# Performance work log

Measured on AMD Instinct MI355X. Metric: run time of the kernel, lower is better.

The kernel has to match this reference:

```python
import jax, jax.numpy as jnp
import numpy as np

N = 50000      # nodes
E = 800000     # edges (avg degree 16)
H = 128        # hidden_channels
F = 128        # num_filters
G = 50         # num_gaussians
L = 6          # num_interactions
CUT = 10.0     # cutoff
H2 = H // 2
OUT = 12


def ssp(x):
    # ShiftedSoftplus: softplus(x) - log(2)
    return jax.nn.softplus(x) - jnp.log(2.0)


def setup_inputs() -> dict:
    key = jax.random.key(0)
    ks = jax.random.split(key, 16)
    s = 0.05
    x_atoms = jax.random.randint(ks[0], (N,), 0, 100)
    edge_index = jax.random.randint(ks[1], (2, E), 0, N)
    edge_attr = jax.random.uniform(ks[2], (E,), minval=0.05, maxval=CUT)
    return {
        "x_atoms": x_atoms,
        "edge_index": edge_index,
        "edge_attr": edge_attr,
        "embedding": jax.random.normal(ks[3], (100, H)) * s,
        # per-interaction stacked params [L, ...]
        "mlp_w1": jax.random.normal(ks[4], (L, G, F)) * s,
        "mlp_b1": jnp.zeros((L, F)),
        "mlp_w2": jax.random.normal(ks[5], (L, F, F)) * s,
        "mlp_b2": jnp.zeros((L, F)),
        "conv1_w": jax.random.normal(ks[6], (L, H, F)) * s,   # CFConv.lin1 (no bias)
        "conv2_w": jax.random.normal(ks[7], (L, F, H)) * s,   # CFConv.lin2
        "conv2_b": jnp.zeros((L, H)),
        "int_lin_w": jax.random.normal(ks[8], (L, H, H)) * s,  # InteractionBlock.lin
        "int_lin_b": jnp.zeros((L, H)),
        # head
        "lin1_w": jax.random.normal(ks[9], (H, H2)) * s,
        "lin1_b": jnp.zeros((H2,)),
        "lin2_w": jax.random.normal(ks[10], (H2, H2)) * s,
        "lin2_b": jnp.zeros((H2,)),
        "readout_w": jax.random.normal(ks[11], (H2, OUT)) * s,
        "readout_b": jnp.zeros((OUT,)),
    }


def reference(x_atoms, edge_index, edge_attr, embedding,
              mlp_w1, mlp_b1, mlp_w2, mlp_b2,
              conv1_w, conv2_w, conv2_b, int_lin_w, int_lin_b,
              lin1_w, lin1_b, lin2_w, lin2_b, readout_w, readout_b):
    h = embedding[x_atoms]  # [N, H]

    # Gaussian smearing of distances -> [E, G]
    offset = jnp.linspace(0.0, CUT, G)
    coeff = -0.5 / (offset[1] - offset[0]) ** 2
    ed = jnp.exp(coeff * (edge_attr[:, None] - offset) ** 2)

    # cosine cutoff weight per edge
    C = 0.5 * (jnp.cos(edge_attr * jnp.pi / CUT) + 1.0)  # [E]

    src = edge_index[0]
    dst = edge_index[1]

    for l in range(L):
        # filter network on expanded distances -> [E, F]
        W = ssp(ed @ mlp_w1[l] + mlp_b1[l]) @ mlp_w2[l] + mlp_b2[l]
        W = W * C[:, None]
        xf = h @ conv1_w[l]                     # [N, F]
        msg = xf[src] * W                        # gather + modulate, [E, F]
        agg = jax.ops.segment_sum(msg, dst, num_segments=N)  # scatter-add, [N, F]
        v = agg @ conv2_w[l] + conv2_b[l]        # [N, H]
        v = ssp(v)
        v = v @ int_lin_w[l] + int_lin_b[l]
        h = h + v                                # residual

    h = ssp(h @ lin1_w + lin1_b)
    h = h @ lin2_w + lin2_b
    h_agg = jnp.sum(h, axis=0, keepdims=True)    # [1, H2]
    return h_agg @ readout_w + readout_b         # [1, OUT]
```

## Files before the change

kernel.cpp:

```cpp
#include <hip/hip_runtime.h>
#include <hip/hip_bf16.h>
#include <math.h>

#define NN 50000
#define EE 800000
#define HH 128
#define FF 128
#define GG 50
#define LL 6
#define H2D 64
#define OUT_DIM 12
#define NK 4096
#define NBLK 782
#define SB 196
#define NBUK 196

typedef __bf16 bf16;
typedef __attribute__((ext_vector_type(8))) __bf16 bf16x8;
typedef __attribute__((ext_vector_type(4))) __bf16 bf16x4;
typedef __attribute__((ext_vector_type(4))) float f32x4;
typedef __attribute__((ext_vector_type(4))) unsigned u32x4;

#define DEV __device__ __forceinline__

DEV float sspf(float x) {
    return fmaxf(x, 0.f) + __logf(1.f + __expf(-fabsf(x))) - 0.69314718055994531f;
}

DEV f32x4 mfma16(bf16x8 a, bf16x8 b, f32x4 c) {
    return __builtin_amdgcn_mfma_f32_16x16x32_bf16(a, b, c, 0, 0, 0);
}

DEV float blo(unsigned u) { return __uint_as_float(u << 16); }
DEV float bhi(unsigned u) { return __uint_as_float(u & 0xffff0000u); }

struct PrepArgs {
    const float *conv1_w, *conv2_w, *int_lin_w, *mlp_w1, *mlp_w2, *lin1_w, *lin2_w;
    bf16 *c1t, *c2t, *ilt, *w1t, *w2t, *l1t, *l2t;
};

__global__ void prep_kernel(PrepArgs p) {
    int j = blockIdx.x;
    const float* src = nullptr; bf16* dst = nullptr; int R = 0, C = 0, K = 0;
    if (j < 30) {
        int l = j / 5, m = j % 5;
        switch (m) {
            case 0: src = p.conv1_w + l * HH * FF;   dst = p.c1t + l * FF * HH;  R = HH; C = FF; K = HH; break;
            case 1: src = p.conv2_w + l * FF * HH;   dst = p.c2t + l * HH * FF;  R = FF; C = HH; K = FF; break;
            case 2: src = p.int_lin_w + l * HH * HH; dst = p.ilt + l * HH * HH;  R = HH; C = HH; K = HH; break;
            case 3: src = p.mlp_w1 + l * GG * FF;    dst = p.w1t + l * FF * 64;  R = GG; C = FF; K = 64; break;
            case 4: src = p.mlp_w2 + l * FF * FF;    dst = p.w2t + l * FF * FF;  R = FF; C = FF; K = FF; break;
        }
    } else if (j == 30) { src = p.lin1_w; dst = p.l1t; R = HH;  C = H2D; K = HH; }
    else                { src = p.lin2_w; dst = p.l2t; R = H2D; C = H2D; K = H2D; }
    int total = C * K;
    for (int idx = threadIdx.x; idx < total; idx += blockDim.x) {
        int c = idx / K, r = idx - c * K;
        dst[idx] = (r < R) ? (bf16)src[r * C + c] : (bf16)0.f;
    }
}

__global__ __launch_bounds__(256) void table_kernel(const bf16* __restrict__ w1t,
                                                    const bf16* __restrict__ w2t,
                                                    const float* __restrict__ mlp_b1,
                                                    const float* __restrict__ mlp_b2,
                                                    bf16* __restrict__ tab) {
    __shared__ bf16 sW1[128 * 72];
    __shared__ bf16 sW2[128 * 136];
    __shared__ bf16 sT1[64 * 136];
    int tid = threadIdx.x;
    int l = blockIdx.x / 65, rb = blockIdx.x % 65;
    const bf16* W1 = w1t + (size_t)l * 128 * 64;
    const bf16* W2 = w2t + (size_t)l * 128 * 128;
    for (int idx = tid * 8; idx < 128 * 64; idx += 2048) {
        int n = idx >> 6, k = idx & 63;
        *(bf16x8*)&sW1[n * 72 + k] = *(const bf16x8*)(W1 + idx);
    }
    for (int idx = tid * 8; idx < 128 * 128; idx += 2048) {
        int n = idx >> 7, k = idx & 127;
        *(bf16x8*)&sW2[n * 136 + k] = *(const bf16x8*)(W2 + idx);
    }
    int w = tid >> 6, lane = tid & 63, ln = lane & 15, kg = lane >> 4;
    int rowt = rb * 64 + w * 16;
    float d1 = (float)min(rowt + ln, NK) * (10.f / NK);
    const float step = 10.f / 49.f;
    const float coeff = -0.5f / (step * step);
    __syncthreads();
    f32x4 acc[8] = {};
#pragma unroll
    for (int k0 = 0; k0 < 64; k0 += 32) {
        bf16x8 a;
#pragma unroll
        for (int jj = 0; jj < 8; jj++) {
            int g = k0 + kg * 8 + jj;
            float diff = d1 - g * step;
            float v = (g < GG) ? __expf(coeff * diff * diff) : 0.f;
            a[jj] = (bf16)v;
        }
#pragma unroll
        for (int t = 0; t < 8; t++) {
            bf16x8 b = *(const bf16x8*)&sW1[(t * 16 + ln) * 72 + k0 + kg * 8];
            acc[t] = mfma16(a, b, acc[t]);
        }
    }
    const float* b1 = mlp_b1 + l * FF;
#pragma unroll
    for (int t = 0; t < 8; t++) {
        int colt = t * 16 + ln;
        float bb = b1[colt];
#pragma unroll
        for (int r = 0; r < 4; r++)
            sT1[(w * 16 + kg * 4 + r) * 136 + colt] = (bf16)sspf(acc[t][r] + bb);
    }
    __syncthreads();
    f32x4 acc2[8] = {};
#pragma unroll
    for (int k0 = 0; k0 < 128; k0 += 32) {
        bf16x8 a = *(const bf16x8*)&sT1[(w * 16 + ln) * 136 + k0 + kg * 8];
#pragma unroll
        for (int t = 0; t < 8; t++) {
            bf16x8 b = *(const bf16x8*)&sW2[(t * 16 + ln) * 136 + k0 + kg * 8];
            acc2[t] = mfma16(a, b, acc2[t]);
        }
    }
    const float* b2 = mlp_b2 + l * FF;
    float Cw[4]; int rrow[4];
#pragma unroll
    for (int r = 0; r < 4; r++) {
        int rr = rowt + kg * 4 + r;
        rrow[r] = rr;
        float dd = (float)min(rr, NK) * (10.f / NK);
        Cw[r] = 0.5f * (cosf(dd * 0.31415926535897932f) + 1.f);
    }
#pragma unroll
    for (int t = 0; t < 8; t++) {
        int colt = t * 16 + ln;
        float bb = b2[colt];
#pragma unroll
        for (int r = 0; r < 4; r++) {
            if (rrow[r] <= NK)
                tab[((size_t)l * (NK + 1) + rrow[r]) * FF + colt] = (bf16)((acc2[t][r] + bb) * Cw[r]);
        }
    }
}

__global__ void hist_kernel(const int* __restrict__ eidx, int* __restrict__ hist) {
    int e = blockIdx.x * 256 + threadIdx.x;
    if (e < EE) atomicAdd(&hist[eidx[EE + e]], 1);
}

__global__ __launch_bounds__(256) void scanA_kernel(const int* __restrict__ hist,
                                                    int* __restrict__ bsum) {
    __shared__ int red[256];
    int t = threadIdx.x;
    int i = blockIdx.x * 256 + t;
    int v = (i < NN) ? hist[i] : 0;
    red[t] = v;
    __syncthreads();
    for (int off = 128; off > 0; off >>= 1) {
        if (t < off) red[t] += red[t + off];
        __syncthreads();
    }
    if (t == 0) bsum[blockIdx.x] = red[0];
}

__global__ __launch_bounds__(256) void scanB_kernel(int* __restrict__ bsum) {
    __shared__ int buf[256];
    int t = threadIdx.x;
    int v = (t < SB) ? bsum[t] : 0;
    buf[t] = v;
    __syncthreads();
    for (int off = 1; off < 256; off <<= 1) {
        int y = (t >= off) ? buf[t - off] : 0;
        __syncthreads();
        buf[t] += y;
        __syncthreads();
    }
    if (t < SB) bsum[t] = buf[t] - v;
}

__global__ __launch_bounds__(256) void scanC_kernel(const int* __restrict__ hist,
                                                    const int* __restrict__ bsum,
                                                    int* __restrict__ rs) {
    __shared__ int buf[256];
    int t = threadIdx.x;
    int i = blockIdx.x * 256 + t;
    int v = (i < NN) ? hist[i] : 0;
    buf[t] = v;
    __syncthreads();
    for (int off = 1; off < 256; off <<= 1) {
        int y = (t >= off) ? buf[t - off] : 0;
        __syncthreads();
        buf[t] += y;
        __syncthreads();
    }
    if (i < NN) rs[i] = buf[t] - v + bsum[blockIdx.x];
}

__global__ void bukinit_kernel(const int* __restrict__ rs, int* __restrict__ bucket_cur) {
    int b = threadIdx.x;
    if (b < NBUK) bucket_cur[b] = rs[b * 256];
}

__global__ __launch_bounds__(256) void scat1_kernel(const float* __restrict__ eattr,
                                                    const int* __restrict__ eidx,
                                                    int* __restrict__ bucket_cur,
                                                    int2* __restrict__ tmp8) {
    __shared__ int cnt[NBUK];
    __shared__ int res[NBUK];
    int t = threadIdx.x;
    for (int i = t; i < NBUK; i += 256) cnt[i] = 0;
    __syncthreads();
    int e0 = blockIdx.x * 4096;
    int pv[16], dd[16], bk[16];
#pragma unroll
    for (int i = 0; i < 16; i++) {
        int e = e0 + i * 256 + t;
        if (e < EE) {
            int d = eidx[EE + e];
            int k = (int)(eattr[e] * ((float)NK / 10.f) + 0.5f);
            k = min(k, NK);
            pv[i] = k | (eidx[e] << 13);
            dd[i] = d;
            bk[i] = d >> 8;
            atomicAdd(&cnt[bk[i]], 1);
        } else bk[i] = -1;
    }
    __syncthreads();
    for (int i = t; i < NBUK; i += 256) {
        int c = cnt[i];
        res[i] = (c > 0) ? atomicAdd(&bucket_cur[i], c) : 0;
        cnt[i] = 0;
    }
    __syncthreads();
#pragma unroll
    for (int i = 0; i < 16; i++) {
        if (bk[i] >= 0) {
            int rank = atomicAdd(&cnt[bk[i]], 1);
            int2 v; v.x = pv[i]; v.y = dd[i];
            tmp8[res[bk[i]] + rank] = v;
        }
    }
}

__global__ __launch_bounds__(256) void scat2_kernel(const int* __restrict__ rs,
                                                    const int2* __restrict__ tmp8,
                                                    int* __restrict__ es) {
    __shared__ int off[256];
    __shared__ int loc[256];
    int b = blockIdx.x, t = threadIdx.x;
    int nb0 = b * 256;
    int nnb = min(256, NN - nb0);
    int base = rs[nb0];
    int end = (nb0 + 256 < NN) ? rs[nb0 + 256] : EE;
    loc[t] = 0;
    if (t < nnb) off[t] = rs[nb0 + t] - base;
    __syncthreads();
    for (int e = base + t; e < end; e += 256) {
        int2 v = tmp8[e];
        int nl = v.y - nb0;
        int rank = atomicAdd(&loc[nl], 1);
        es[base + off[nl] + rank] = v.x;
    }
}

__global__ void embed_kernel(const int* __restrict__ x_atoms, const float* __restrict__ emb,
                             bf16* __restrict__ hb) {
    int idx = blockIdx.x * blockDim.x + threadIdx.x;
    if (idx >= NN * 16) return;
    int n = idx >> 4, ch = idx & 15;
    int a = x_atoms[n];
    const float* ep = emb + a * HH + ch * 8;
    f32x4 v0 = *(const f32x4*)ep;
    f32x4 v1 = *(const f32x4*)(ep + 4);
    bf16x8 vb;
#pragma unroll
    for (int q = 0; q < 4; q++) { vb[q] = (bf16)v0[q]; vb[q + 4] = (bf16)v1[q]; }
    *(bf16x8*)(hb + n * HH + ch * 8) = vb;
}

__global__ __launch_bounds__(256) void xf_kernel(const bf16* __restrict__ hb,
                                                 const bf16* __restrict__ c1t,
                                                 bf16* __restrict__ xf) {
    __shared__ bf16 sB[128 * 136];
    int tid = threadIdx.x;
    for (int idx = tid * 8; idx < 128 * 128; idx += 2048) {
        int n = idx >> 7, k = idx & 127;
        *(bf16x8*)&sB[n * 136 + k] = *(const bf16x8*)(c1t + idx);
    }
    int w = tid >> 6, lane = tid & 63, ln = lane & 15, kg = lane >> 4;
    int rowt = blockIdx.x * 64 + w * 16;
    int arow = min(rowt + ln, NN - 1);
    __syncthreads();
    f32x4 acc[8] = {};
#pragma unroll
    for (int k0 = 0; k0 < 128; k0 += 32) {
        bf16x8 a = *(const bf16x8*)(hb + arow * HH + k0 + kg * 8);
#pragma unroll
        for (int t = 0; t < 8; t++) {
            bf16x8 b = *(const bf16x8*)&sB[(t * 16 + ln) * 136 + k0 + kg * 8];
            acc[t] = mfma16(a, b, acc[t]);
        }
    }
#pragma unroll
    for (int t = 0; t < 8; t++) {
        int colt = t * 16 + ln;
#pragma unroll
        for (int r = 0; r < 4; r++) {
            int orow = rowt + kg * 4 + r;
            if (orow < NN) xf[orow * FF + colt] = (bf16)acc[t][r];
        }
    }
}

__global__ __launch_bounds__(256) void edge_kernel(const int* __restrict__ es,
                                                   const int* __restrict__ rs,
                                                   const int* __restrict__ hist,
                                                   const bf16* __restrict__ xf,
                                                   const bf16* __restrict__ tab,
                                                   bf16* __restrict__ aggb) {
    int tid = threadIdx.x;
    int w = tid >> 6, lane = tid & 63;
    int q = lane >> 4, cl = lane & 15;
    int n = blockIdx.x * 4 + w;
    int start = rs[n], deg = hist[n];
    float a0 = 0.f, a1 = 0.f, a2 = 0.f, a3 = 0.f;
    float a4 = 0.f, a5 = 0.f, a6 = 0.f, a7 = 0.f;
    for (int base = 0; base < deg; base += 64) {
        int cnt = min(deg - base, 64);
        int pv = (lane < cnt) ? es[start + base + lane] : 0;
        int iters = (cnt + 3) >> 2;
#pragma unroll 4
        for (int j = 0; j < iters; j++) {
            int jj = 4 * j + q;
            bool valid = jj < cnt;
            int v = __shfl(pv, jj);
            int k = v & 8191;
            int s = v >> 13;
            u32x4 tp = *(const u32x4*)(tab + (size_t)k * FF + 8 * cl);
            u32x4 xu = *(const u32x4*)(xf + (size_t)s * FF + 8 * cl);
            unsigned t0 = valid ? tp.x : 0u;
            unsigned t1 = valid ? tp.y : 0u;
            unsigned t2 = valid ? tp.z : 0u;
            unsigned t3 = valid ? tp.w : 0u;
            a0 = fmaf(blo(t0), blo(xu.x), a0);
            a1 = fmaf(bhi(t0), bhi(xu.x), a1);
            a2 = fmaf(blo(t1), blo(xu.y), a2);
            a3 = fmaf(bhi(t1), bhi(xu.y), a3);
            a4 = fmaf(blo(t2), blo(xu.z), a4);
            a5 = fmaf(bhi(t2), bhi(xu.z), a5);
            a6 = fmaf(blo(t3), blo(xu.w), a6);
            a7 = fmaf(bhi(t3), bhi(xu.w), a7);
        }
    }
    a0 += __shfl_xor(a0, 16); a0 += __shfl_xor(a0, 32);
    a1 += __shfl_xor(a1, 16); a1 += __shfl_xor(a1, 32);
    a2 += __shfl_xor(a2, 16); a2 += __shfl_xor(a2, 32);
    a3 += __shfl_xor(a3, 16); a3 += __shfl_xor(a3, 32);
    a4 += __shfl_xor(a4, 16); a4 += __shfl_xor(a4, 32);
    a5 += __shfl_xor(a5, 16); a5 += __shfl_xor(a5, 32);
    a6 += __shfl_xor(a6, 16); a6 += __shfl_xor(a6, 32);
    a7 += __shfl_xor(a7, 16); a7 += __shfl_xor(a7, 32);
    if (q == 0) {
        bf16x8 pk;
        pk[0] = (bf16)a0; pk[1] = (bf16)a1; pk[2] = (bf16)a2; pk[3] = (bf16)a3;
        pk[4] = (bf16)a4; pk[5] = (bf16)a5; pk[6] = (bf16)a6; pk[7] = (bf16)a7;
        *(bf16x8*)(aggb + (size_t)n * FF + 8 * cl) = pk;
    }
}

__global__ __launch_bounds__(256) void update_kernel(const bf16* __restrict__ aggb,
                                                     const bf16* __restrict__ c2t,
                                                     const float* __restrict__ c2b,
                                                     const bf16* __restrict__ ilt,
                                                     const float* __restrict__ ilb,
                                                     bf16* __restrict__ hb,
                                                     const bf16* __restrict__ c1n,
                                                     bf16* __restrict__ xf_out,
                                                     const bf16* __restrict__ l1t,
                                                     const float* __restrict__ l1b,
                                                     const bf16* __restrict__ l2t,
                                                     const float* __restrict__ l2b,
                                                     float* __restrict__ partial) {
    __shared__ bf16 sB[128 * 136];
    __shared__ bf16 sT[64 * 136];
    int tid = threadIdx.x;
    int w = tid >> 6, lane = tid & 63, ln = lane & 15, kg = lane >> 4;
    int rowt = blockIdx.x * 64 + w * 16;
    int nrow = rowt + ln;
    int arow = min(nrow, NN - 1);
    bool rowok = nrow < NN;
    bf16x4 hpre[8];
#pragma unroll
    for (int t = 0; t < 8; t++)
        hpre[t] = *(const bf16x4*)(hb + (size_t)arow * HH + t * 16 + kg * 4);
    for (int idx = tid * 8; idx < 128 * 128; idx += 2048) {
        int n = idx >> 7, k = idx & 127;
        *(bf16x8*)&sB[n * 136 + k] = *(const bf16x8*)(c2t + idx);
    }
    __syncthreads();
    f32x4 acc[8] = {};
#pragma unroll
    for (int k0 = 0; k0 < 128; k0 += 32) {
        bf16x8 bfrag = *(const bf16x8*)(aggb + (size_t)arow * FF + k0 + kg * 8);
#pragma unroll
        for (int t = 0; t < 8; t++) {
            bf16x8 afrag = *(const bf16x8*)&sB[(t * 16 + ln) * 136 + k0 + kg * 8];
            acc[t] = mfma16(afrag, bfrag, acc[t]);
        }
    }
#pragma unroll
    for (int t = 0; t < 8; t++) {
        f32x4 bb = *(const f32x4*)(c2b + t * 16 + kg * 4);
        bf16x4 pk;
#pragma unroll
        for (int r = 0; r < 4; r++) pk[r] = (bf16)sspf(acc[t][r] + bb[r]);
        *(bf16x4*)&sT[(w * 16 + ln) * 136 + t * 16 + kg * 4] = pk;
    }
    __syncthreads();
    for (int idx = tid * 8; idx < 128 * 128; idx += 2048) {
        int n = idx >> 7, k = idx & 127;
        *(bf16x8*)&sB[n * 136 + k] = *(const bf16x8*)(ilt + idx);
    }
    __syncthreads();
    f32x4 acc2[8] = {};
#pragma unroll
    for (int k0 = 0; k0 < 128; k0 += 32) {
        bf16x8 bfrag = *(const bf16x8*)&sT[(w * 16 + ln) * 136 + k0 + kg * 8];
#pragma unroll
        for (int t = 0; t < 8; t++) {
            bf16x8 afrag = *(const bf16x8*)&sB[(t * 16 + ln) * 136 + k0 + kg * 8];
            acc2[t] = mfma16(afrag, bfrag, acc2[t]);
        }
    }
    bool is_last = (c1n == nullptr);
#pragma unroll
    for (int t = 0; t < 8; t++) {
        f32x4 bb = *(const f32x4*)(ilb + t * 16 + kg * 4);
        bf16x4 pk;
#pragma unroll
        for (int r = 0; r < 4; r++)
            pk[r] = (bf16)((float)hpre[t][r] + acc2[t][r] + bb[r]);
        if (rowok && !is_last) *(bf16x4*)(hb + (size_t)nrow * HH + t * 16 + kg * 4) = pk;
        *(bf16x4*)&sT[(w * 16 + ln) * 136 + t * 16 + kg * 4] = pk;
    }
    if (!is_last) {
        __syncthreads();
        for (int idx = tid * 8; idx < 128 * 128; idx += 2048) {
            int n = idx >> 7, k = idx & 127;
            *(bf16x8*)&sB[n * 136 + k] = *(const bf16x8*)(c1n + idx);
        }
        __syncthreads();
        f32x4 acc3[8] = {};
#pragma unroll
        for (int k0 = 0; k0 < 128; k0 += 32) {
            bf16x8 bfrag = *(const bf16x8*)&sT[(w * 16 + ln) * 136 + k0 + kg * 8];
#pragma unroll
            for (int t = 0; t < 8; t++) {
                bf16x8 afrag = *(const bf16x8*)&sB[(t * 16 + ln) * 136 + k0 + kg * 8];
                acc3[t] = mfma16(afrag, bfrag, acc3[t]);
            }
        }
#pragma unroll
        for (int t = 0; t < 8; t++) {
            bf16x4 pk;
#pragma unroll
            for (int r = 0; r < 4; r++) pk[r] = (bf16)acc3[t][r];
            if (rowok) *(bf16x4*)(xf_out + (size_t)nrow * FF + t * 16 + kg * 4) = pk;
        }
    } else {
        __syncthreads();
        for (int idx = tid * 8; idx < 64 * 128; idx += 2048) {
            int n = idx >> 7, k = idx & 127;
            *(bf16x8*)&sB[n * 136 + k] = *(const bf16x8*)(l1t + idx);
        }
        __syncthreads();
        f32x4 acch[4] = {};
#pragma unroll
        for (int k0 = 0; k0 < 128; k0 += 32) {
            bf16x8 a = *(const bf16x8*)&sT[(w * 16 + ln) * 136 + k0 + kg * 8];
#pragma unroll
            for (int t = 0; t < 4; t++) {
                bf16x8 b = *(const bf16x8*)&sB[(t * 16 + ln) * 136 + k0 + kg * 8];
                acch[t] = mfma16(a, b, acch[t]);
            }
        }
#pragma unroll
        for (int t = 0; t < 4; t++) {
            int colt = t * 16 + ln;
            float bb = l1b[colt];
#pragma unroll
            for (int r = 0; r < 4; r++)
                sT[(w * 16 + kg * 4 + r) * 136 + colt] = (bf16)sspf(acch[t][r] + bb);
        }
        __syncthreads();
        for (int idx = tid * 8; idx < 64 * 64; idx += 2048) {
            int n = idx >> 6, k = idx & 63;
            *(bf16x8*)&sB[n * 136 + k] = *(const bf16x8*)(l2t + idx);
        }
        __syncthreads();
        f32x4 acc2h[4] = {};
#pragma unroll
        for (int k0 = 0; k0 < 64; k0 += 32) {
            bf16x8 a = *(const bf16x8*)&sT[(w * 16 + ln) * 136 + k0 + kg * 8];
#pragma unroll
            for (int t = 0; t < 4; t++) {
                bf16x8 b = *(const bf16x8*)&sB[(t * 16 + ln) * 136 + k0 + kg * 8];
                acc2h[t] = mfma16(a, b, acc2h[t]);
            }
        }
        __syncthreads();
        float* sPart = (float*)sT;
#pragma unroll
        for (int t = 0; t < 4; t++) {
            int colt = t * 16 + ln;
            float bb = l2b[colt];
            float v = 0.f;
#pragma unroll
            for (int r = 0; r < 4; r++) {
                int orow = rowt + kg * 4 + r;
                if (orow < NN) v += acc2h[t][r] + bb;
            }
            v += __shfl_xor(v, 16);
            v += __shfl_xor(v, 32);
            if (kg == 0) sPart[w * 64 + colt] = v;
        }
        __syncthreads();
        if (tid < 64) {
            float s = sPart[tid] + sPart[64 + tid] + sPart[128 + tid] + sPart[192 + tid];
            partial[blockIdx.x * 64 + tid] = s;
        }
    }
}

__global__ __launch_bounds__(64) void final_kernel(const float* __restrict__ partial,
                                                   const float* __restrict__ rw,
                                                   const float* __restrict__ rb,
                                                   float* __restrict__ out) {
    __shared__ float sv[64];
    int j = threadIdx.x;
    float s = 0.f;
    for (int b = 0; b < NBLK; b++) s += partial[b * 64 + j];
    sv[j] = s;
    __syncthreads();
    if (j < OUT_DIM) {
        float o = rb[j];
        for (int i = 0; i < H2D; i++) o += sv[i] * rw[i * OUT_DIM + j];
        out[j] = o;
    }
}

extern "C" void kernel_launch(void* const* d_in, const int* in_sizes, int n_in,
                              void* d_out, int out_size, void* d_ws, size_t ws_size,
                              hipStream_t stream) {
    const int*   x_atoms    = (const int*)d_in[0];
    const int*   edge_index = (const int*)d_in[1];
    const float* edge_attr  = (const float*)d_in[2];
    const float* embedding  = (const float*)d_in[3];
    const float* mlp_w1     = (const float*)d_in[4];
    const float* mlp_b1     = (const float*)d_in[5];
    const float* mlp_w2     = (const float*)d_in[6];
    const float* mlp_b2     = (const float*)d_in[7];
    const float* conv1_w    = (const float*)d_in[8];
    const float* conv2_w    = (const float*)d_in[9];
    const float* conv2_b    = (const float*)d_in[10];
    const float* int_lin_w  = (const float*)d_in[11];
    const float* int_lin_b  = (const float*)d_in[12];
    const float* lin1_w     = (const float*)d_in[13];
    const float* lin1_b     = (const float*)d_in[14];
    const float* lin2_w     = (const float*)d_in[15];
    const float* lin2_b     = (const float*)d_in[16];
    const float* readout_w  = (const float*)d_in[17];
    const float* readout_b  = (const float*)d_in[18];

    char* ws = (char*)d_ws;
    bf16*  hb      = (bf16*)(ws + 0);
    bf16*  xfA     = (bf16*)(ws + 12800000);
    bf16*  xfB     = (bf16*)(ws + 25600000);
    bf16*  aggb    = (bf16*)(ws + 38400000);
    float* partial = (float*)(ws + 51200000);
    size_t wb = 51400192;
    bf16* c1t = (bf16*)(ws + wb);
    bf16* c2t = (bf16*)(ws + wb + 196608);
    bf16* ilt = (bf16*)(ws + wb + 393216);
    bf16* w1t = (bf16*)(ws + wb + 589824);
    bf16* w2t = (bf16*)(ws + wb + 688128);
    bf16* l1t = (bf16*)(ws + wb + 884736);
    bf16* l2t = (bf16*)(ws + wb + 901120);
    int*   d_hist = (int*)(ws + 52309504);
    int*   d_rs   = (int*)(ws + 52509504);
    int*   d_bcur = (int*)(ws + 52709504);
    int*   d_bsum = (int*)(ws + 52710528);
    int*   d_es   = (int*)(ws + 52711552);
    bf16*  tab    = (bf16*)(ws + 55911552);
    int2*  d_tmp8 = (int2*)(ws + 62204544);

    PrepArgs pa = { conv1_w, conv2_w, int_lin_w, mlp_w1, mlp_w2, lin1_w, lin2_w,
                    c1t, c2t, ilt, w1t, w2t, l1t, l2t };
    prep_kernel<<<32, 256, 0, stream>>>(pa);
    table_kernel<<<LL * 65, 256, 0, stream>>>(w1t, w2t, mlp_b1, mlp_b2, tab);
    embed_kernel<<<NN * 16 / 256, 256, 0, stream>>>(x_atoms, embedding, hb);

    hipMemsetAsync(d_hist, 0, NN * 4, stream);
    hist_kernel<<<(EE + 255) / 256, 256, 0, stream>>>(edge_index, d_hist);
    scanA_kernel<<<SB, 256, 0, stream>>>(d_hist, d_bsum);
    scanB_kernel<<<1, 256, 0, stream>>>(d_bsum);
    scanC_kernel<<<SB, 256, 0, stream>>>(d_hist, d_bsum, d_rs);
    bukinit_kernel<<<1, 256, 0, stream>>>(d_rs, d_bcur);
    scat1_kernel<<<NBUK, 256, 0, stream>>>(edge_attr, edge_index, d_bcur, d_tmp8);
    scat2_kernel<<<NBUK, 256, 0, stream>>>(d_rs, d_tmp8, d_es);

    xf_kernel<<<NBLK, 256, 0, stream>>>(hb, c1t, xfA);
    bf16* xf_in = xfA;
    bf16* xf_out = xfB;
    for (int l = 0; l < LL; l++) {
        edge_kernel<<<NN / 4, 256, 0, stream>>>(d_es, d_rs, d_hist, xf_in,
                                                tab + (size_t)l * (NK + 1) * FF, aggb);
        const bf16* c1n = (l + 1 < LL) ? (c1t + (size_t)(l + 1) * FF * HH) : nullptr;
        update_kernel<<<NBLK, 256, 0, stream>>>(aggb, c2t + (size_t)l * HH * FF,
                                                conv2_b + l * HH,
                                                ilt + (size_t)l * HH * HH, int_lin_b + l * HH,
                                                hb, c1n, xf_out,
                                                l1t, lin1_b, l2t, lin2_b, partial);
        bf16* tmp = xf_in; xf_in = xf_out; xf_out = tmp;
    }
    final_kernel<<<1, 64, 0, stream>>>(partial, readout_w, readout_b, (float*)d_out);
}
```

Measured before the change: 587.5 us.

## Remap edge kernel to 16 lanes per node and fuse embed into xf

The edge aggregation kernel now gives each node 16 threads, each walking the full edge list serially with unroll 2, in place of a 64-lane wavefront that split edges four ways and reduced with cross-lane shuffles. This removes the shuffle-based reduction and the padded, masked iterations for low-degree nodes, and packs 16 nodes into each block. The cost is a serial dependency chain per thread over about 16 edges, which relies on other wavefronts to hide latency. Separately, the embedding lookup is fused into the first xf GEMM kernel, and the bucket-cursor init is folded into scanC, which removes two launches.

After: 594.1 us. Within noise of the previous version (+1.1%).

```diff
diff --git a/kernel.cpp b/kernel.cpp
--- a/kernel.cpp
+++ b/kernel.cpp
@@ -181,7 +181,8 @@
 
 __global__ __launch_bounds__(256) void scanC_kernel(const int* __restrict__ hist,
                                                     const int* __restrict__ bsum,
-                                                    int* __restrict__ rs) {
+                                                    int* __restrict__ rs,
+                                                    int* __restrict__ bucket_cur) {
     __shared__ int buf[256];
     int t = threadIdx.x;
     int i = blockIdx.x * 256 + t;
@@ -194,12 +195,11 @@
         buf[t] += y;
         __syncthreads();
     }
-    if (i < NN) rs[i] = buf[t] - v + bsum[blockIdx.x];
-}
-
-__global__ void bukinit_kernel(const int* __restrict__ rs, int* __restrict__ bucket_cur) {
-    int b = threadIdx.x;
-    if (b < NBUK) bucket_cur[b] = rs[b * 256];
+    if (i < NN) {
+        int ex = buf[t] - v + bsum[blockIdx.x];
+        rs[i] = ex;
+        if ((i & 255) == 0) bucket_cur[i >> 8] = ex;
+    }
 }
 
 __global__ __launch_bounds__(256) void scat1_kernel(const float* __restrict__ eattr,
@@ -264,24 +264,11 @@
     }
 }
 
-__global__ void embed_kernel(const int* __restrict__ x_atoms, const float* __restrict__ emb,
-                             bf16* __restrict__ hb) {
-    int idx = blockIdx.x * blockDim.x + threadIdx.x;
-    if (idx >= NN * 16) return;
-    int n = idx >> 4, ch = idx & 15;
-    int a = x_atoms[n];
-    const float* ep = emb + a * HH + ch * 8;
-    f32x4 v0 = *(const f32x4*)ep;
-    f32x4 v1 = *(const f32x4*)(ep + 4);
-    bf16x8 vb;
-#pragma unroll
-    for (int q = 0; q < 4; q++) { vb[q] = (bf16)v0[q]; vb[q + 4] = (bf16)v1[q]; }
-    *(bf16x8*)(hb + n * HH + ch * 8) = vb;
-}
-
-__global__ __launch_bounds__(256) void xf_kernel(const bf16* __restrict__ hb,
-                                                 const bf16* __restrict__ c1t,
-                                                 bf16* __restrict__ xf) {
+__global__ __launch_bounds__(256) void xf0_kernel(const int* __restrict__ x_atoms,
+                                                  const float* __restrict__ emb,
+                                                  const bf16* __restrict__ c1t,
+                                                  bf16* __restrict__ hb,
+                                                  bf16* __restrict__ xf) {
     __shared__ bf16 sB[128 * 136];
     int tid = threadIdx.x;
     for (int idx = tid * 8; idx < 128 * 128; idx += 2048) {
@@ -290,12 +277,21 @@
     }
     int w = tid >> 6, lane = tid & 63, ln = lane & 15, kg = lane >> 4;
     int rowt = blockIdx.x * 64 + w * 16;
-    int arow = min(rowt + ln, NN - 1);
+    int nrow = rowt + ln;
+    int arow = min(nrow, NN - 1);
+    bool rowok = nrow < NN;
+    int atom = x_atoms[arow];
     __syncthreads();
     f32x4 acc[8] = {};
 #pragma unroll
     for (int k0 = 0; k0 < 128; k0 += 32) {
-        bf16x8 a = *(const bf16x8*)(hb + arow * HH + k0 + kg * 8);
+        const float* ep = emb + (size_t)atom * HH + k0 + kg * 8;
+        f32x4 u0 = *(const f32x4*)ep;
+        f32x4 u1 = *(const f32x4*)(ep + 4);
+        bf16x8 a;
+#pragma unroll
+        for (int q = 0; q < 4; q++) { a[q] = (bf16)u0[q]; a[q + 4] = (bf16)u1[q]; }
+        if (rowok) *(bf16x8*)(hb + (size_t)nrow * HH + k0 + kg * 8) = a;
 #pragma unroll
         for (int t = 0; t < 8; t++) {
             bf16x8 b = *(const bf16x8*)&sB[(t * 16 + ln) * 136 + k0 + kg * 8];
@@ -320,53 +316,32 @@
                                                    const bf16* __restrict__ tab,
                                                    bf16* __restrict__ aggb) {
     int tid = threadIdx.x;
-    int w = tid >> 6, lane = tid & 63;
-    int q = lane >> 4, cl = lane & 15;
-    int n = blockIdx.x * 4 + w;
+    int qq = tid >> 4;
+    int cl = tid & 15;
+    int n = blockIdx.x * 16 + qq;
     int start = rs[n], deg = hist[n];
     float a0 = 0.f, a1 = 0.f, a2 = 0.f, a3 = 0.f;
     float a4 = 0.f, a5 = 0.f, a6 = 0.f, a7 = 0.f;
-    for (int base = 0; base < deg; base += 64) {
-        int cnt = min(deg - base, 64);
-        int pv = (lane < cnt) ? es[start + base + lane] : 0;
-        int iters = (cnt + 3) >> 2;
-#pragma unroll 4
-        for (int j = 0; j < iters; j++) {
-            int jj = 4 * j + q;
-            bool valid = jj < cnt;
-            int v = __shfl(pv, jj);
-            int k = v & 8191;
-            int s = v >> 13;
-            u32x4 tp = *(const u32x4*)(tab + (size_t)k * FF + 8 * cl);
-            u32x4 xu = *(const u32x4*)(xf + (size_t)s * FF + 8 * cl);
-            unsigned t0 = valid ? tp.x : 0u;
-            unsigned t1 = valid ? tp.y : 0u;
-            unsigned t2 = valid ? tp.z : 0u;
-            unsigned t3 = valid ? tp.w : 0u;
-            a0 = fmaf(blo(t0), blo(xu.x), a0);
-            a1 = fmaf(bhi(t0), bhi(xu.x), a1);
-            a2 = fmaf(blo(t1), blo(xu.y), a2);
-            a3 = fmaf(bhi(t1), bhi(xu.y), a3);
-            a4 = fmaf(blo(t2), blo(xu.z), a4);
-            a5 = fmaf(bhi(t2), bhi(xu.z), a5);
-            a6 = fmaf(blo(t3), blo(xu.w), a6);
-            a7 = fmaf(bhi(t3), bhi(xu.w), a7);
-        }
-    }
-    a0 += __shfl_xor(a0, 16); a0 += __shfl_xor(a0, 32);
-    a1 += __shfl_xor(a1, 16); a1 += __shfl_xor(a1, 32);
-    a2 += __shfl_xor(a2, 16); a2 += __shfl_xor(a2, 32);
-    a3 += __shfl_xor(a3, 16); a3 += __shfl_xor(a3, 32);
-    a4 += __shfl_xor(a4, 16); a4 += __shfl_xor(a4, 32);
-    a5 += __shfl_xor(a5, 16); a5 += __shfl_xor(a5, 32);
-    a6 += __shfl_xor(a6, 16); a6 += __shfl_xor(a6, 32);
-    a7 += __shfl_xor(a7, 16); a7 += __shfl_xor(a7, 32);
-    if (q == 0) {
-        bf16x8 pk;
-        pk[0] = (bf16)a0; pk[1] = (bf16)a1; pk[2] = (bf16)a2; pk[3] = (bf16)a3;
-        pk[4] = (bf16)a4; pk[5] = (bf16)a5; pk[6] = (bf16)a6; pk[7] = (bf16)a7;
-        *(bf16x8*)(aggb + (size_t)n * FF + 8 * cl) = pk;
-    }
+#pragma unroll 2
+    for (int i = 0; i < deg; i++) {
+        int v = es[start + i];
+        int k = v & 8191;
+        int s = v >> 13;
+        u32x4 tp = *(const u32x4*)(tab + (size_t)k * FF + 8 * cl);
+        u32x4 xu = *(const u32x4*)(xf + (size_t)s * FF + 8 * cl);
+        a0 = fmaf(blo(tp.x), blo(xu.x), a0);
+        a1 = fmaf(bhi(tp.x), bhi(xu.x), a1);
+        a2 = fmaf(blo(tp.y), blo(xu.y), a2);
+        a3 = fmaf(bhi(tp.y), bhi(xu.y), a3);
+        a4 = fmaf(blo(tp.z), blo(xu.z), a4);
+        a5 = fmaf(bhi(tp.z), bhi(xu.z), a5);
+        a6 = fmaf(blo(tp.w), blo(xu.w), a6);
+        a7 = fmaf(bhi(tp.w), bhi(xu.w), a7);
+    }
+    bf16x8 pk;
+    pk[0] = (bf16)a0; pk[1] = (bf16)a1; pk[2] = (bf16)a2; pk[3] = (bf16)a3;
+    pk[4] = (bf16)a4; pk[5] = (bf16)a5; pk[6] = (bf16)a6; pk[7] = (bf16)a7;
+    *(bf16x8*)(aggb + (size_t)n * FF + 8 * cl) = pk;
 }
 
 __global__ __launch_bounds__(256) void update_kernel(const bf16* __restrict__ aggb,
@@ -599,23 +574,21 @@
                     c1t, c2t, ilt, w1t, w2t, l1t, l2t };
     prep_kernel<<<32, 256, 0, stream>>>(pa);
     table_kernel<<<LL * 65, 256, 0, stream>>>(w1t, w2t, mlp_b1, mlp_b2, tab);
-    embed_kernel<<<NN * 16 / 256, 256, 0, stream>>>(x_atoms, embedding, hb);
 
     hipMemsetAsync(d_hist, 0, NN * 4, stream);
     hist_kernel<<<(EE + 255) / 256, 256, 0, stream>>>(edge_index, d_hist);
     scanA_kernel<<<SB, 256, 0, stream>>>(d_hist, d_bsum);
     scanB_kernel<<<1, 256, 0, stream>>>(d_bsum);
-    scanC_kernel<<<SB, 256, 0, stream>>>(d_hist, d_bsum, d_rs);
-    bukinit_kernel<<<1, 256, 0, stream>>>(d_rs, d_bcur);
+    scanC_kernel<<<SB, 256, 0, stream>>>(d_hist, d_bsum, d_rs, d_bcur);
     scat1_kernel<<<NBUK, 256, 0, stream>>>(edge_attr, edge_index, d_bcur, d_tmp8);
     scat2_kernel<<<NBUK, 256, 0, stream>>>(d_rs, d_tmp8, d_es);
 
-    xf_kernel<<<NBLK, 256, 0, stream>>>(hb, c1t, xfA);
+    xf0_kernel<<<NBLK, 256, 0, stream>>>(x_atoms, embedding, c1t, hb, xfA);
     bf16* xf_in = xfA;
     bf16* xf_out = xfB;
     for (int l = 0; l < LL; l++) {
-        edge_kernel<<<NN / 4, 256, 0, stream>>>(d_es, d_rs, d_hist, xf_in,
-                                                tab + (size_t)l * (NK + 1) * FF, aggb);
+        edge_kernel<<<NN / 16, 256, 0, stream>>>(d_es, d_rs, d_hist, xf_in,
+                                                 tab + (size_t)l * (NK + 1) * FF, aggb);
         const bf16* c1n = (l + 1 < LL) ? (c1t + (size_t)(l + 1) * FF * HH) : nullptr;
         update_kernel<<<NBLK, 256, 0, stream>>>(aggb, c2t + (size_t)l * HH * FF,
                                                 conv2_b + l * HH,
```

## Merge setup kernels into one cooperative persistent kernel with grid syncs

Applied to the files above, without the earlier changes.

Replaces the chain of roughly a dozen setup launches (weight prep, filter table, embedding, histogram, scans, bucket scatter, first xf GEMM) with a single cooperative kernel of 392 blocks that uses grid.sync between phases. Independent work such as the table GEMM and the scan partials, or the xf GEMM and the block-sum scan, runs in the same phase. The embedding lookup is folded into the xf GEMM, so the separate hb round trip is gone. The cost is several grid-wide barriers, about 70KB of static shared memory per block that limits residency, and a cooperative launch requirement.

After: 878.8 us. +49.6%, slower.

```diff
diff --git a/kernel.cpp b/kernel.cpp
--- a/kernel.cpp
+++ b/kernel.cpp
@@ -1,6 +1,9 @@
 #include <hip/hip_runtime.h>
+#include <hip/hip_cooperative_groups.h>
 #include <hip/hip_bf16.h>
 #include <math.h>
+
+namespace cg = cooperative_groups;
 
 #define NN 50000
 #define EE 800000
@@ -14,6 +17,7 @@
 #define NBLK 782
 #define SB 196
 #define NBUK 196
+#define NB 392
 
 typedef __bf16 bf16;
 typedef __attribute__((ext_vector_type(8))) __bf16 bf16x8;
@@ -34,44 +38,44 @@
 DEV float blo(unsigned u) { return __uint_as_float(u << 16); }
 DEV float bhi(unsigned u) { return __uint_as_float(u & 0xffff0000u); }
 
-struct PrepArgs {
+struct SetupArgs {
     const float *conv1_w, *conv2_w, *int_lin_w, *mlp_w1, *mlp_w2, *lin1_w, *lin2_w;
     bf16 *c1t, *c2t, *ilt, *w1t, *w2t, *l1t, *l2t;
+    const float *mlp_b1, *mlp_b2;
+    const int* edge_index; const float* edge_attr;
+    int* hist; int* bsum; int* rs; int* bcur;
+    int2* tmp8; int* es;
+    const int* x_atoms; const float* emb;
+    bf16* tab; bf16* hb; bf16* xf;
 };
 
-__global__ void prep_kernel(PrepArgs p) {
-    int j = blockIdx.x;
+DEV void prep_job(const SetupArgs& a, int j, int tid) {
     const float* src = nullptr; bf16* dst = nullptr; int R = 0, C = 0, K = 0;
     if (j < 30) {
         int l = j / 5, m = j % 5;
         switch (m) {
-            case 0: src = p.conv1_w + l * HH * FF;   dst = p.c1t + l * FF * HH;  R = HH; C = FF; K = HH; break;
-            case 1: src = p.conv2_w + l * FF * HH;   dst = p.c2t + l * HH * FF;  R = FF; C = HH; K = FF; break;
-            case 2: src = p.int_lin_w + l * HH * HH; dst = p.ilt + l * HH * HH;  R = HH; C = HH; K = HH; break;
-            case 3: src = p.mlp_w1 + l * GG * FF;    dst = p.w1t + l * FF * 64;  R = GG; C = FF; K = 64; break;
-            case 4: src = p.mlp_w2 + l * FF * FF;    dst = p.w2t + l * FF * FF;  R = FF; C = FF; K = FF; break;
-        }
-    } else if (j == 30) { src = p.lin1_w; dst = p.l1t; R = HH;  C = H2D; K = HH; }
-    else                { src = p.lin2_w; dst = p.l2t; R = H2D; C = H2D; K = H2D; }
+            case 0: src = a.conv1_w + l * HH * FF;   dst = a.c1t + l * FF * HH;  R = HH; C = FF; K = HH; break;
+            case 1: src = a.conv2_w + l * FF * HH;   dst = a.c2t + l * HH * FF;  R = FF; C = HH; K = FF; break;
+            case 2: src = a.int_lin_w + l * HH * HH; dst = a.ilt + l * HH * HH;  R = HH; C = HH; K = HH; break;
+            case 3: src = a.mlp_w1 + l * GG * FF;    dst = a.w1t + l * FF * 64;  R = GG; C = FF; K = 64; break;
+            case 4: src = a.mlp_w2 + l * FF * FF;    dst = a.w2t + l * FF * FF;  R = FF; C = FF; K = FF; break;
+        }
+    } else if (j == 30) { src = a.lin1_w; dst = a.l1t; R = HH;  C = H2D; K = HH; }
+    else                { src = a.lin2_w; dst = a.l2t; R = H2D; C = H2D; K = H2D; }
     int total = C * K;
-    for (int idx = threadIdx.x; idx < total; idx += blockDim.x) {
+    for (int idx = tid; idx < total; idx += 256) {
         int c = idx / K, r = idx - c * K;
         dst[idx] = (r < R) ? (bf16)src[r * C + c] : (bf16)0.f;
     }
 }
 
-__global__ __launch_bounds__(256) void table_kernel(const bf16* __restrict__ w1t,
-                                                    const bf16* __restrict__ w2t,
-                                                    const float* __restrict__ mlp_b1,
-                                                    const float* __restrict__ mlp_b2,
-                                                    bf16* __restrict__ tab) {
-    __shared__ bf16 sW1[128 * 72];
-    __shared__ bf16 sW2[128 * 136];
-    __shared__ bf16 sT1[64 * 136];
-    int tid = threadIdx.x;
-    int l = blockIdx.x / 65, rb = blockIdx.x % 65;
-    const bf16* W1 = w1t + (size_t)l * 128 * 64;
-    const bf16* W2 = w2t + (size_t)l * 128 * 128;
+DEV void table_job(const SetupArgs& a, int job, char* smem, int tid) {
+    bf16* sW1 = (bf16*)smem;
+    bf16* sW2 = (bf16*)(smem + 18432);
+    bf16* sT1 = (bf16*)(smem + 53248);
+    int l = job / 65, rb = job % 65;
+    const bf16* W1 = a.w1t + (size_t)l * 128 * 64;
+    const bf16* W2 = a.w2t + (size_t)l * 128 * 128;
     for (int idx = tid * 8; idx < 128 * 64; idx += 2048) {
         int n = idx >> 6, k = idx & 63;
         *(bf16x8*)&sW1[n * 72 + k] = *(const bf16x8*)(W1 + idx);
@@ -89,21 +93,21 @@
     f32x4 acc[8] = {};
 #pragma unroll
     for (int k0 = 0; k0 < 64; k0 += 32) {
-        bf16x8 a;
+        bf16x8 av;
 #pragma unroll
         for (int jj = 0; jj < 8; jj++) {
             int g = k0 + kg * 8 + jj;
             float diff = d1 - g * step;
             float v = (g < GG) ? __expf(coeff * diff * diff) : 0.f;
-            a[jj] = (bf16)v;
+            av[jj] = (bf16)v;
         }
 #pragma unroll
         for (int t = 0; t < 8; t++) {
             bf16x8 b = *(const bf16x8*)&sW1[(t * 16 + ln) * 72 + k0 + kg * 8];
-            acc[t] = mfma16(a, b, acc[t]);
-        }
-    }
-    const float* b1 = mlp_b1 + l * FF;
+            acc[t] = mfma16(av, b, acc[t]);
+        }
+    }
+    const float* b1 = a.mlp_b1 + l * FF;
 #pragma unroll
     for (int t = 0; t < 8; t++) {
         int colt = t * 16 + ln;
@@ -116,14 +120,14 @@
     f32x4 acc2[8] = {};
 #pragma unroll
     for (int k0 = 0; k0 < 128; k0 += 32) {
-        bf16x8 a = *(const bf16x8*)&sT1[(w * 16 + ln) * 136 + k0 + kg * 8];
+        bf16x8 av = *(const bf16x8*)&sT1[(w * 16 + ln) * 136 + k0 + kg * 8];
 #pragma unroll
         for (int t = 0; t < 8; t++) {
             bf16x8 b = *(const bf16x8*)&sW2[(t * 16 + ln) * 136 + k0 + kg * 8];
-            acc2[t] = mfma16(a, b, acc2[t]);
-        }
-    }
-    const float* b2 = mlp_b2 + l * FF;
+            acc2[t] = mfma16(av, b, acc2[t]);
+        }
+    }
+    const float* b2 = a.mlp_b2 + l * FF;
     float Cw[4]; int rrow[4];
 #pragma unroll
     for (int r = 0; r < 4; r++) {
@@ -139,167 +143,38 @@
 #pragma unroll
         for (int r = 0; r < 4; r++) {
             if (rrow[r] <= NK)
-                tab[((size_t)l * (NK + 1) + rrow[r]) * FF + colt] = (bf16)((acc2[t][r] + bb) * Cw[r]);
-        }
-    }
-}
-
-__global__ void hist_kernel(const int* __restrict__ eidx, int* __restrict__ hist) {
-    int e = blockIdx.x * 256 + threadIdx.x;
-    if (e < EE) atomicAdd(&hist[eidx[EE + e]], 1);
-}
-
-__global__ __launch_bounds__(256) void scanA_kernel(const int* __restrict__ hist,
-                                                    int* __restrict__ bsum) {
-    __shared__ int red[256];
-    int t = threadIdx.x;
-    int i = blockIdx.x * 256 + t;
-    int v = (i < NN) ? hist[i] : 0;
-    red[t] = v;
-    __syncthreads();
-    for (int off = 128; off > 0; off >>= 1) {
-        if (t < off) red[t] += red[t + off];
-        __syncthreads();
-    }
-    if (t == 0) bsum[blockIdx.x] = red[0];
-}
-
-__global__ __launch_bounds__(256) void scanB_kernel(int* __restrict__ bsum) {
-    __shared__ int buf[256];
-    int t = threadIdx.x;
-    int v = (t < SB) ? bsum[t] : 0;
-    buf[t] = v;
-    __syncthreads();
-    for (int off = 1; off < 256; off <<= 1) {
-        int y = (t >= off) ? buf[t - off] : 0;
-        __syncthreads();
-        buf[t] += y;
-        __syncthreads();
-    }
-    if (t < SB) bsum[t] = buf[t] - v;
-}
-
-__global__ __launch_bounds__(256) void scanC_kernel(const int* __restrict__ hist,
-                                                    const int* __restrict__ bsum,
-                                                    int* __restrict__ rs) {
-    __shared__ int buf[256];
-    int t = threadIdx.x;
-    int i = blockIdx.x * 256 + t;
-    int v = (i < NN) ? hist[i] : 0;
-    buf[t] = v;
-    __syncthreads();
-    for (int off = 1; off < 256; off <<= 1) {
-        int y = (t >= off) ? buf[t - off] : 0;
-        __syncthreads();
-        buf[t] += y;
-        __syncthreads();
-    }
-    if (i < NN) rs[i] = buf[t] - v + bsum[blockIdx.x];
-}
-
-__global__ void bukinit_kernel(const int* __restrict__ rs, int* __restrict__ bucket_cur) {
-    int b = threadIdx.x;
-    if (b < NBUK) bucket_cur[b] = rs[b * 256];
-}
-
-__global__ __launch_bounds__(256) void scat1_kernel(const float* __restrict__ eattr,
-                                                    const int* __restrict__ eidx,
-                                                    int* __restrict__ bucket_cur,
-                                                    int2* __restrict__ tmp8) {
-    __shared__ int cnt[NBUK];
-    __shared__ int res[NBUK];
-    int t = threadIdx.x;
-    for (int i = t; i < NBUK; i += 256) cnt[i] = 0;
-    __syncthreads();
-    int e0 = blockIdx.x * 4096;
-    int pv[16], dd[16], bk[16];
-#pragma unroll
-    for (int i = 0; i < 16; i++) {
-        int e = e0 + i * 256 + t;
-        if (e < EE) {
-            int d = eidx[EE + e];
-            int k = (int)(eattr[e] * ((float)NK / 10.f) + 0.5f);
-            k = min(k, NK);
-            pv[i] = k | (eidx[e] << 13);
-            dd[i] = d;
-            bk[i] = d >> 8;
-            atomicAdd(&cnt[bk[i]], 1);
-        } else bk[i] = -1;
-    }
-    __syncthreads();
-    for (int i = t; i < NBUK; i += 256) {
-        int c = cnt[i];
-        res[i] = (c > 0) ? atomicAdd(&bucket_cur[i], c) : 0;
-        cnt[i] = 0;
-    }
-    __syncthreads();
-#pragma unroll
-    for (int i = 0; i < 16; i++) {
-        if (bk[i] >= 0) {
-            int rank = atomicAdd(&cnt[bk[i]], 1);
-            int2 v; v.x = pv[i]; v.y = dd[i];
-            tmp8[res[bk[i]] + rank] = v;
-        }
-    }
-}
-
-__global__ __launch_bounds__(256) void scat2_kernel(const int* __restrict__ rs,
-                                                    const int2* __restrict__ tmp8,
-                                                    int* __restrict__ es) {
-    __shared__ int off[256];
-    __shared__ int loc[256];
-    int b = blockIdx.x, t = threadIdx.x;
-    int nb0 = b * 256;
-    int nnb = min(256, NN - nb0);
-    int base = rs[nb0];
-    int end = (nb0 + 256 < NN) ? rs[nb0 + 256] : EE;
-    loc[t] = 0;
-    if (t < nnb) off[t] = rs[nb0 + t] - base;
-    __syncthreads();
-    for (int e = base + t; e < end; e += 256) {
-        int2 v = tmp8[e];
-        int nl = v.y - nb0;
-        int rank = atomicAdd(&loc[nl], 1);
-        es[base + off[nl] + rank] = v.x;
-    }
-}
-
-__global__ void embed_kernel(const int* __restrict__ x_atoms, const float* __restrict__ emb,
-                             bf16* __restrict__ hb) {
-    int idx = blockIdx.x * blockDim.x + threadIdx.x;
-    if (idx >= NN * 16) return;
-    int n = idx >> 4, ch = idx & 15;
-    int a = x_atoms[n];
-    const float* ep = emb + a * HH + ch * 8;
-    f32x4 v0 = *(const f32x4*)ep;
-    f32x4 v1 = *(const f32x4*)(ep + 4);
-    bf16x8 vb;
-#pragma unroll
-    for (int q = 0; q < 4; q++) { vb[q] = (bf16)v0[q]; vb[q + 4] = (bf16)v1[q]; }
-    *(bf16x8*)(hb + n * HH + ch * 8) = vb;
-}
-
-__global__ __launch_bounds__(256) void xf_kernel(const bf16* __restrict__ hb,
-                                                 const bf16* __restrict__ c1t,
-                                                 bf16* __restrict__ xf) {
-    __shared__ bf16 sB[128 * 136];
-    int tid = threadIdx.x;
+                a.tab[((size_t)l * (NK + 1) + rrow[r]) * FF + colt] = (bf16)((acc2[t][r] + bb) * Cw[r]);
+        }
+    }
+}
+
+DEV void xf0_job(const SetupArgs& a, int job, char* smem, int tid) {
+    bf16* sB = (bf16*)smem;
     for (int idx = tid * 8; idx < 128 * 128; idx += 2048) {
         int n = idx >> 7, k = idx & 127;
-        *(bf16x8*)&sB[n * 136 + k] = *(const bf16x8*)(c1t + idx);
+        *(bf16x8*)&sB[n * 136 + k] = *(const bf16x8*)(a.c1t + idx);
     }
     int w = tid >> 6, lane = tid & 63, ln = lane & 15, kg = lane >> 4;
-    int rowt = blockIdx.x * 64 + w * 16;
-    int arow = min(rowt + ln, NN - 1);
+    int rowt = job * 64 + w * 16;
+    int nrow = rowt + ln;
+    int arow = min(nrow, NN - 1);
+    bool rowok = nrow < NN;
+    int atom = a.x_atoms[arow];
     __syncthreads();
     f32x4 acc[8] = {};
 #pragma unroll
     for (int k0 = 0; k0 < 128; k0 += 32) {
-        bf16x8 a = *(const bf16x8*)(hb + arow * HH + k0 + kg * 8);
+        const float* ep = a.emb + (size_t)atom * HH + k0 + kg * 8;
+        f32x4 u0 = *(const f32x4*)ep;
+        f32x4 u1 = *(const f32x4*)(ep + 4);
+        bf16x8 av;
+#pragma unroll
+        for (int q = 0; q < 4; q++) { av[q] = (bf16)u0[q]; av[q + 4] = (bf16)u1[q]; }
+        if (rowok) *(bf16x8*)(a.hb + (size_t)nrow * HH + k0 + kg * 8) = av;
 #pragma unroll
         for (int t = 0; t < 8; t++) {
             bf16x8 b = *(const bf16x8*)&sB[(t * 16 + ln) * 136 + k0 + kg * 8];
-            acc[t] = mfma16(a, b, acc[t]);
+            acc[t] = mfma16(av, b, acc[t]);
         }
     }
 #pragma unroll
@@ -308,7 +183,132 @@
 #pragma unroll
         for (int r = 0; r < 4; r++) {
             int orow = rowt + kg * 4 + r;
-            if (orow < NN) xf[orow * FF + colt] = (bf16)acc[t][r];
+            if (orow < NN) a.xf[orow * FF + colt] = (bf16)acc[t][r];
+        }
+    }
+}
+
+__global__ __launch_bounds__(256) void setup_kernel(SetupArgs a) {
+    cg::grid_group grid = cg::this_grid();
+    __shared__ __align__(16) char smem[70656];
+    __shared__ int aux[768];
+    int tid = threadIdx.x, bid = blockIdx.x;
+    int gtid = bid * 256 + tid;
+    const int gsz = NB * 256;
+
+    for (int i = gtid; i < NN; i += gsz) a.hist[i] = 0;
+    if (bid < 32) prep_job(a, bid, tid);
+    grid.sync();
+
+    for (int e = gtid; e < EE; e += gsz) atomicAdd(&a.hist[a.edge_index[EE + e]], 1);
+    grid.sync();
+
+    if (bid < SB) {
+        int* red = aux;
+        int i = bid * 256 + tid;
+        int v = (i < NN) ? a.hist[i] : 0;
+        red[tid] = v;
+        __syncthreads();
+        for (int off = 128; off > 0; off >>= 1) {
+            if (tid < off) red[tid] += red[tid + off];
+            __syncthreads();
+        }
+        if (tid == 0) a.bsum[bid] = red[0];
+        __syncthreads();
+    }
+    if (bid < 390) table_job(a, bid, smem, tid);
+    grid.sync();
+
+    if (bid == 0) {
+        int* buf = aux;
+        int v = (tid < SB) ? a.bsum[tid] : 0;
+        buf[tid] = v;
+        __syncthreads();
+        for (int off = 1; off < 256; off <<= 1) {
+            int y = (tid >= off) ? buf[tid - off] : 0;
+            __syncthreads();
+            buf[tid] += y;
+            __syncthreads();
+        }
+        if (tid < SB) a.bsum[tid] = buf[tid] - v;
+    }
+    for (int job = bid; job < NBLK; job += NB) {
+        __syncthreads();
+        xf0_job(a, job, smem, tid);
+    }
+    grid.sync();
+
+    if (bid < SB) {
+        int* buf = aux;
+        int i = bid * 256 + tid;
+        int v = (i < NN) ? a.hist[i] : 0;
+        buf[tid] = v;
+        __syncthreads();
+        for (int off = 1; off < 256; off <<= 1) {
+            int y = (tid >= off) ? buf[tid - off] : 0;
+            __syncthreads();
+            buf[tid] += y;
+            __syncthreads();
+        }
+        if (i < NN) {
+            int ex = buf[tid] - v + a.bsum[bid];
+            a.rs[i] = ex;
+            if (tid == 0) a.bcur[i >> 8] = ex;
+        }
+    }
+    grid.sync();
+
+    {
+        int* cnt = aux; int* res = aux + 196;
+        if (tid < NBUK) cnt[tid] = 0;
+        __syncthreads();
+        int e0 = bid * 2048;
+        int pv[8], dd[8], bk[8];
+#pragma unroll
+        for (int i = 0; i < 8; i++) {
+            int e = e0 + i * 256 + tid;
+            if (e < EE) {
+                int d = a.edge_index[EE + e];
+                int k = (int)(a.edge_attr[e] * ((float)NK / 10.f) + 0.5f);
+                k = min(k, NK);
+                pv[i] = k | (a.edge_index[e] << 13);
+                dd[i] = d;
+                bk[i] = d >> 8;
+                atomicAdd(&cnt[bk[i]], 1);
+            } else bk[i] = -1;
+        }
+        __syncthreads();
+        if (tid < NBUK) {
+            int c = cnt[tid];
+            res[tid] = (c > 0) ? atomicAdd(&a.bcur[tid], c) : 0;
+            cnt[tid] = 0;
+        }
+        __syncthreads();
+#pragma unroll
+        for (int i = 0; i < 8; i++) {
+            if (bk[i] >= 0) {
+                int rank = atomicAdd(&cnt[bk[i]], 1);
+                int2 v; v.x = pv[i]; v.y = dd[i];
+                a.tmp8[res[bk[i]] + rank] = v;
+            }
+        }
+    }
+    grid.sync();
+
+    if (bid < NBUK) {
+        int* off_ = aux; int* loc = aux + 256;
+        int nb0 = bid * 256;
+        int nnb = min(256, NN - nb0);
+        int base = a.rs[nb0];
+        int end = (nb0 + 256 < NN) ? a.rs[nb0 + 256] : EE;
+        loc[tid] = 0;
+        if (tid < nnb) off_[tid] = a.rs[nb0 + tid] - base;
+        __syncthreads();
+        for (int e = base + tid; e < end; e += 256) {
+            int2 v = a.tmp8[e];
+            int nl = v.y - nb0;
+            int rank = atomicAdd(&loc[nl], 1);
+            a.es[base + off_[nl] + rank] = v.x;
         }
     }
 }
@@ -595,22 +595,20 @@
     bf16*  tab    = (bf16*)(ws + 55911552);
     int2*  d_tmp8 = (int2*)(ws + 62204544);
 
-    PrepArgs pa = { conv1_w, conv2_w, int_lin_w, mlp_w1, mlp_w2, lin1_w, lin2_w,
-                    c1t, c2t, ilt, w1t, w2t, l1t, l2t };
-    prep_kernel<<<32, 256, 0, stream>>>(pa);
-    table_kernel<<<LL * 65, 256, 0, stream>>>(w1t, w2t, mlp_b1, mlp_b2, tab);
-    embed_kernel<<<NN * 16 / 256, 256, 0, stream>>>(x_atoms, embedding, hb);
-
-    hipMemsetAsync(d_hist, 0, NN * 4, stream);
-    hist_kernel<<<(EE + 255) / 256, 256, 0, stream>>>(edge_index, d_hist);
-    scanA_kernel<<<SB, 256, 0, stream>>>(d_hist, d_bsum);
-    scanB_kernel<<<1, 256, 0, stream>>>(d_bsum);
-    scanC_kernel<<<SB, 256, 0, stream>>>(d_hist, d_bsum, d_rs);
-    bukinit_kernel<<<1, 256, 0, stream>>>(d_rs, d_bcur);
-    scat1_kernel<<<NBUK, 256, 0, stream>>>(edge_attr, edge_index, d_bcur, d_tmp8);
-    scat2_kernel<<<NBUK, 256, 0, stream>>>(d_rs, d_tmp8, d_es);
-
-    xf_kernel<<<NBLK, 256, 0, stream>>>(hb, c1t, xfA);
+    SetupArgs sa;
+    sa.conv1_w = conv1_w; sa.conv2_w = conv2_w; sa.int_lin_w = int_lin_w;
+    sa.mlp_w1 = mlp_w1; sa.mlp_w2 = mlp_w2; sa.lin1_w = lin1_w; sa.lin2_w = lin2_w;
+    sa.c1t = c1t; sa.c2t = c2t; sa.ilt = ilt; sa.w1t = w1t; sa.w2t = w2t;
+    sa.l1t = l1t; sa.l2t = l2t;
+    sa.mlp_b1 = mlp_b1; sa.mlp_b2 = mlp_b2;
+    sa.edge_index = edge_index; sa.edge_attr = edge_attr;
+    sa.hist = d_hist; sa.bsum = d_bsum; sa.rs = d_rs; sa.bcur = d_bcur;
+    sa.tmp8 = d_tmp8; sa.es = d_es;
+    sa.x_atoms = x_atoms; sa.emb = embedding;
+    sa.tab = tab; sa.hb = hb; sa.xf = xfA;
+    void* kp[] = { (void*)&sa };
+    hipLaunchCooperativeKernel((const void*)setup_kernel, dim3(NB), dim3(256), kp, 0, stream);
+
     bf16* xf_in = xfA;
     bf16* xf_out = xfB;
     for (int l = 0; l < LL; l++) {
```
